# Kernel optimization log

Hardware: AMD Instinct MI355X
Metric: run time of the kernel (lower is better)

Reference implementation:

```python
import jax, jax.numpy as jnp
import numpy as np

N, NB, EU, ED, EB = 40000, 60000, 200000, 200000, 120000
D, H = 256, 256
BN_EPS = 1e-5


def _bn(x, g, b):
    # training-mode BatchNorm1d over the cell dimension (biased variance)
    mu = jnp.mean(x, axis=0)
    var = jnp.mean((x - mu) ** 2, axis=0)
    return g * (x - mu) * jax.lax.rsqrt(var + BN_EPS) + b


def _mlp(x, W1, b1, g1, c1, W2, b2, g2, c2):
    # update nn: Linear -> BN -> ReLU -> Linear -> BN -> ReLU
    h = jax.nn.relu(_bn(x @ W1 + b1, g1, c1))
    return jax.nn.relu(_bn(h @ W2 + b2, g2, c2))


def _forward(x, up_attr, down_attr, boundary_attr, Wmu, bmu, Wmd, bmd,
             W1u, b1u, g1u, c1u, W2u, b2u, g2u, c2u,
             W1d, b1d, g1d, c1d, W2d, b2d, g2d, c2d,
             W1b, b1b, g1b, c1b, W2b, b2b, g2b, c2b,
             Wc, bc, gc, cc, eps1, eps2, eps3,
             up_index, down_index, boundary_index):
    n, d = x.shape
    # msg_up_nn = ReLU(Linear(cat[x_j, up_attr])); split W to avoid materializing cat
    mu = jax.nn.relu(x[up_index[0]] @ Wmu[:d] + up_attr @ Wmu[d:] + bmu)
    agg_up = jax.ops.segment_sum(mu, up_index[1], num_segments=n)
    md = jax.nn.relu(x[down_index[0]] @ Wmd[:d] + down_attr @ Wmd[d:] + bmd)
    agg_down = jax.ops.segment_sum(md, down_index[1], num_segments=n)
    # msg_boundaries_nn is identity: gather boundary cell features, sum to targets
    agg_bnd = jax.ops.segment_sum(boundary_attr[boundary_index[0]], boundary_index[1], num_segments=n)
    out_up = _mlp(agg_up + (1.0 + eps1) * x, W1u, b1u, g1u, c1u, W2u, b2u, g2u, c2u)
    out_down = _mlp(agg_down + (1.0 + eps2) * x, W1d, b1d, g1d, c1d, W2d, b2d, g2d, c2d)
    out_bnd = _mlp(agg_bnd + (1.0 + eps3) * x, W1b, b1b, g1b, c1b, W2b, b2b, g2b, c2b)
    comb = jnp.concatenate([out_up, out_down, out_bnd], axis=-1)
    return jax.nn.relu(_bn(comb @ Wc + bc, gc, cc))


def setup_inputs() -> dict:
    key = jax.random.key(0)
    ks = iter(jax.random.split(key, 64))

    def nrm(shape, scale=1.0):
        return jax.random.normal(next(ks), shape, dtype=jnp.float32) * scale

    inp = {}
    inp['x'] = nrm((N, D))
    inp['up_attr'] = nrm((EU, D))
    inp['down_attr'] = nrm((ED, D))
    inp['boundary_attr'] = nrm((NB, D))
    s_msg = 1.0 / np.sqrt(2 * D)
    inp['Wmu'] = nrm((2 * D, D), s_msg); inp['bmu'] = jnp.zeros((D,), jnp.float32)
    inp['Wmd'] = nrm((2 * D, D), s_msg); inp['bmd'] = jnp.zeros((D,), jnp.float32)
    s1, s2 = 1.0 / np.sqrt(D), 1.0 / np.sqrt(H)
    for t in ('u', 'd', 'b'):
        inp['W1' + t] = nrm((D, H), s1); inp['b1' + t] = jnp.zeros((H,), jnp.float32)
        inp['g1' + t] = jnp.ones((H,), jnp.float32); inp['c1' + t] = jnp.zeros((H,), jnp.float32)
        inp['W2' + t] = nrm((H, H), s2); inp['b2' + t] = jnp.zeros((H,), jnp.float32)
        inp['g2' + t] = jnp.ones((H,), jnp.float32); inp['c2' + t] = jnp.zeros((H,), jnp.float32)
    inp['Wc'] = nrm((3 * H, H), 1.0 / np.sqrt(3 * H)); inp['bc'] = jnp.zeros((H,), jnp.float32)
    inp['gc'] = jnp.ones((H,), jnp.float32); inp['cc'] = jnp.zeros((H,), jnp.float32)
    inp['eps1'] = jnp.zeros((1,), jnp.float32)
    inp['eps2'] = jnp.zeros((1,), jnp.float32)
    inp['eps3'] = jnp.zeros((1,), jnp.float32)
    inp['up_index'] = jax.random.randint(next(ks), (2, EU), 0, N)
    inp['down_index'] = jax.random.randint(next(ks), (2, ED), 0, N)
    bsrc = jax.random.randint(next(ks), (EB,), 0, NB)
    btgt = jax.random.randint(next(ks), (EB,), 0, N)
    inp['boundary_index'] = jnp.stack([bsrc, btgt], axis=0)
    return inp


def reference(x, up_attr, down_attr, boundary_attr, Wmu, bmu, Wmd, bmd,
              W1u, b1u, g1u, c1u, W2u, b2u, g2u, c2u,
              W1d, b1d, g1d, c1d, W2d, b2d, g2d, c2d,
              W1b, b1b, g1b, c1b, W2b, b2b, g2b, c2b,
              Wc, bc, gc, cc, eps1, eps2, eps3,
              up_index, down_index, boundary_index):
    return _forward(x, up_attr, down_attr, boundary_attr, Wmu, bmu, Wmd, bmd,
                    W1u, b1u, g1u, c1u, W2u, b2u, g2u, c2u,
                    W1d, b1d, g1d, c1d, W2d, b2d, g2d, c2d,
                    W1b, b1b, g1b, c1b, W2b, b2b, g2b, c2b,
                    Wc, bc, gc, cc, eps1, eps2, eps3,
                    up_index, down_index, boundary_index)
```

## Files before the change

kernel.cpp:

```cpp
#include <hip/hip_runtime.h>
#include <hip/hip_bf16.h>
#include <stdint.h>

#define NCELL 40000
#define EUE   200000
#define EDE   200000
#define EBE   120000
#define NM    ((size_t)NCELL * 256)

typedef __attribute__((ext_vector_type(8))) short bf16x8;
typedef __attribute__((ext_vector_type(4))) float f32x4;

__device__ __forceinline__ uint16_t f2bf(float f) {
  union { float f; uint32_t u; } v; v.f = f;
  uint32_t u = v.u;
  u += 0x7fffu + ((u >> 16) & 1u);
  return (uint16_t)(u >> 16);
}

struct WArgs {
  const float* src[11];
  uint16_t*    dst[11];
  int          K[11];
};

__global__ void k_wconv(WArgs a) {
  int m = blockIdx.z;
  int K = a.K[m];
  int k0 = blockIdx.x * 32;
  if (k0 >= K) return;
  int n0 = blockIdx.y * 32;
  __shared__ float t[32][33];
  int tx = threadIdx.x, ty = threadIdx.y;
  const float* src = a.src[m];
  for (int i = ty; i < 32; i += 8)
    t[i][tx] = src[(size_t)(k0 + i) * 256 + n0 + tx];
  __syncthreads();
  uint16_t* dst = a.dst[m];
  for (int i = ty; i < 32; i += 8)
    dst[(size_t)(n0 + i) * K + k0 + tx] = f2bf(t[tx][i]);
}

__global__ void k_count(const int* __restrict__ tgt, int* __restrict__ cnt, int E) {
  int i = blockIdx.x * 256 + threadIdx.x;
  if (i < E) atomicAdd(&cnt[tgt[i]], 1);
}

struct ScanArgs { const int* cnt[3]; int* offs[3]; int* head[3]; };

__global__ void k_scan(ScanArgs a) {
  int s = blockIdx.x;
  const int n = NCELL;
  const int* cnt = a.cnt[s];
  int* offs = a.offs[s];
  int* head = a.head[s];
  __shared__ int buf[1024];
  __shared__ int carry;
  int tid = threadIdx.x;
  if (tid == 0) carry = 0;
  __syncthreads();
  for (int base = 0; base < n; base += 1024) {
    int i = base + tid;
    int v = (i < n) ? cnt[i] : 0;
    buf[tid] = v;
    __syncthreads();
    for (int d = 1; d < 1024; d <<= 1) {
      int t = (tid >= d) ? buf[tid - d] : 0;
      __syncthreads();
      buf[tid] += t;
      __syncthreads();
    }
    int excl = carry + buf[tid] - v;
    if (i < n) { offs[i] = excl; head[i] = excl; }
    __syncthreads();
    if (tid == 1023) carry += buf[1023];
    __syncthreads();
  }
  if (tid == 0) offs[n] = carry;
}

__global__ void k_fill(const int* __restrict__ src, const int* __restrict__ tgt,
                       int* __restrict__ head, int* __restrict__ perm,
                       int* __restrict__ psrc, int E) {
  int e = blockIdx.x * 256 + threadIdx.x;
  if (e < E) {
    int p = atomicAdd(&head[tgt[e]], 1);
    perm[p] = e;
    psrc[p] = src[e];
  }
}

__global__ void k_segsum(const float* __restrict__ MSG, const int* __restrict__ offs,
                         const int* __restrict__ perm, const float* __restrict__ x,
                         const float* __restrict__ eps, float* __restrict__ out) {
  int t = blockIdx.x * 4 + threadIdx.y;
  int c = threadIdx.x * 4;
  int s = offs[t], e = offs[t + 1];
  float sE = 1.f + *eps;
  float4 xa = *(const float4*)(x + (size_t)t * 256 + c);
  float a0 = xa.x * sE, a1 = xa.y * sE, a2 = xa.z * sE, a3 = xa.w * sE;
  int j = s;
  for (; j + 1 < e; j += 2) {
    int r0 = perm[j], r1 = perm[j + 1];
    float4 v0 = *(const float4*)(MSG + (size_t)r0 * 256 + c);
    float4 v1 = *(const float4*)(MSG + (size_t)r1 * 256 + c);
    a0 += v0.x + v1.x; a1 += v0.y + v1.y; a2 += v0.z + v1.z; a3 += v0.w + v1.w;
  }
  if (j < e) {
    int r0 = perm[j];
    float4 v0 = *(const float4*)(MSG + (size_t)r0 * 256 + c);
    a0 += v0.x; a1 += v0.y; a2 += v0.z; a3 += v0.w;
  }
  *(float4*)(out + (size_t)t * 256 + c) = make_float4(a0, a1, a2, a3);
}

__global__ void k_bgather(const float* __restrict__ battr, const int* __restrict__ offs,
                          const int* __restrict__ psrc, const float* __restrict__ x,
                          const float* __restrict__ eps, float* __restrict__ out) {
  int t = blockIdx.x * 4 + threadIdx.y;
  int c = threadIdx.x * 4;
  int s = offs[t], e = offs[t + 1];
  float sE = 1.f + *eps;
  float4 xa = *(const float4*)(x + (size_t)t * 256 + c);
  float a0 = xa.x * sE, a1 = xa.y * sE, a2 = xa.z * sE, a3 = xa.w * sE;
  int j = s;
  for (; j + 1 < e; j += 2) {
    int r0 = psrc[j], r1 = psrc[j + 1];
    float4 v0 = *(const float4*)(battr + (size_t)r0 * 256 + c);
    float4 v1 = *(const float4*)(battr + (size_t)r1 * 256 + c);
    a0 += v0.x + v1.x; a1 += v0.y + v1.y; a2 += v0.z + v1.z; a3 += v0.w + v1.w;
  }
  if (j < e) {
    int r0 = psrc[j];
    float4 v0 = *(const float4*)(battr + (size_t)r0 * 256 + c);
    a0 += v0.x; a1 += v0.y; a2 += v0.z; a3 += v0.w;
  }
  *(float4*)(out + (size_t)t * 256 + c) = make_float4(a0, a1, a2, a3);
}

__global__ void k_bnrelu(const float* __restrict__ Y, const float* __restrict__ s12,
                         const float* __restrict__ g, const float* __restrict__ cb,
                         float* __restrict__ out, int ldo) {
  int i = blockIdx.x * 256 + threadIdx.x;
  int c = (i & 63) * 4;
  size_t row = (size_t)(i >> 6);
  const float invN = 1.f / (float)NCELL;
  float4 v = *(const float4*)(Y + row * 256 + c);
  float vv[4] = {v.x, v.y, v.z, v.w};
  float o[4];
#pragma unroll
  for (int k = 0; k < 4; k++) {
    float mean = s12[c + k] * invN;
    float var  = s12[256 + c + k] * invN - mean * mean;
    float sc = g[c + k] * rsqrtf(var + 1e-5f);
    float sh = cb[c + k] - mean * sc;
    o[k] = fmaxf(vv[k] * sc + sh, 0.f);
  }
  *(float4*)(out + row * (size_t)ldo + c) = make_float4(o[0], o[1], o[2], o[3]);
}

struct CCArgs { const float* g[3]; const float* c[3]; float* Gg; float* Gc; };
__global__ void k_concat(CCArgs a) {
  int t = blockIdx.x, i = threadIdx.x;
  a.Gg[t * 256 + i] = a.g[t][i];
  a.Gc[t * 256 + i] = a.c[t][i];
}

template <int MODE, int FUSEBN>
__global__ __launch_bounds__(256)
void k_gemm(const float* __restrict__ A, const uint16_t* __restrict__ Bt, int K,
            const float* __restrict__ bias, float* __restrict__ C,
            float* __restrict__ stats, float* __restrict__ statsq,
            const float* __restrict__ bnS, const float* __restrict__ bnG,
            const float* __restrict__ bnC, const int* __restrict__ srcIdx,
            const float* __restrict__ XT, int M, int gx) {
  __shared__ uint16_t Al[128 * 32];
  __shared__ uint16_t Bl[128 * 32];
  const int tid = threadIdx.x;
  int id = blockIdx.x;
  int body2 = (gx & ~7) * 2;
  int m0, n0;
  if (id < body2) {
    int g = id >> 4, j = id & 15;
    m0 = ((g << 3) + (j & 7)) * 128;
    n0 = (j >> 3) * 128;
  } else {
    int r = id - body2, rem = gx & 7;
    m0 = ((gx & ~7) + (r % rem)) * 128;
    n0 = (r / rem) * 128;
  }
  const int lane = tid & 63;
  const int wave = tid >> 6;
  const int wr = (wave >> 1) * 64;
  const int wc = (wave & 1) * 64;
  const int lm = lane & 15;
  const int lq = lane >> 4;

  f32x4 acc[4][4];
#pragma unroll
  for (int i = 0; i < 4; i++)
#pragma unroll
    for (int j = 0; j < 4; j++)
      acc[i][j] = f32x4{0.f, 0.f, 0.f, 0.f};

  const int arow = tid >> 3;
  const int acol = (tid & 7) * 4;

  int pidx[4];
#pragma unroll
  for (int rr = 0; rr < 4; rr++) {
    int gr = m0 + arow + rr * 32;
    pidx[rr] = (gr < M) ? gr : -1;
  }

  const float invN = 1.f / (float)NCELL;
  for (int kt = 0; kt < K; kt += 32) {
    float sc[4], sh[4];
    if (FUSEBN) {
#pragma unroll
      for (int k2 = 0; k2 < 4; k2++) {
        int col = kt + acol + k2;
        float mean = bnS[col] * invN;
        float var  = bnS[K + col] * invN - mean * mean;
        float s = bnG[col] * rsqrtf(var + 1e-5f);
        sc[k2] = s; sh[k2] = bnC[col] - mean * s;
      }
    }
#pragma unroll
    for (int rr = 0; rr < 4; rr++) {
      int r = arow + rr * 32;
      float4 v = make_float4(0.f, 0.f, 0.f, 0.f);
      if (pidx[rr] >= 0) {
        const float* ap;
        if (MODE == 2) {
          int ct = kt + acol;
          ap = A + (size_t)(ct >> 8) * NM + (size_t)pidx[rr] * 256 + (ct & 255);
        } else {
          ap = A + (size_t)pidx[rr] * 256 + kt + acol;
        }
        v = *(const float4*)ap;
      }
      if (FUSEBN) {
        v.x = fmaxf(v.x * sc[0] + sh[0], 0.f);
        v.y = fmaxf(v.y * sc[1] + sh[1], 0.f);
        v.z = fmaxf(v.z * sc[2] + sh[2], 0.f);
        v.w = fmaxf(v.w * sc[3] + sh[3], 0.f);
      }
      union { uint16_t h[4]; uint2 u; } p;
      p.h[0] = f2bf(v.x); p.h[1] = f2bf(v.y); p.h[2] = f2bf(v.z); p.h[3] = f2bf(v.w);
      *(uint2*)(Al + r * 32 + acol) = p.u;
    }
#pragma unroll
    for (int ss = 0; ss < 2; ss++) {
      int j = tid + ss * 256;
      int row = j >> 2, kp = (j & 3) * 8;
      uint4 bv = *(const uint4*)(Bt + (size_t)(n0 + row) * K + kt + kp);
      *(uint4*)(Bl + row * 32 + kp) = bv;
    }
    __syncthreads();
    bf16x8 af[4], bfr[4];
#pragma unroll
    for (int i = 0; i < 4; i++)
      af[i] = *(const bf16x8*)(Al + (wr + 16 * i + lm) * 32 + lq * 8);
#pragma unroll
    for (int j = 0; j < 4; j++)
      bfr[j] = *(const bf16x8*)(Bl + (wc + 16 * j + lm) * 32 + lq * 8);
#pragma unroll
    for (int i = 0; i < 4; i++)
#pragma unroll
      for (int j = 0; j < 4; j++)
        acc[i][j] = __builtin_amdgcn_mfma_f32_16x16x32_bf16(af[i], bfr[j], acc[i][j], 0, 0, 0);
    __syncthreads();
  }

  const int cb0 = n0 + wc + lm;
  float bj[4];
#pragma unroll
  for (int j = 0; j < 4; j++) bj[j] = bias ? bias[cb0 + 16 * j] : 0.f;

  if (MODE == 1) {
#pragma unroll
    for (int i = 0; i < 4; i++) {
      int rbase = m0 + wr + 16 * i + lq * 4;
#pragma unroll
      for (int r = 0; r < 4; r++) {
        int row = rbase + r;
        if (row < M) {
          int sr = srcIdx[row];
          const float* xr = XT + (size_t)sr * 256;
#pragma unroll
          for (int j = 0; j < 4; j++) {
            float v = acc[i][j][r] + xr[cb0 + 16 * j] + bj[j];
            C[(size_t)row * 256 + cb0 + 16 * j] = fmaxf(v, 0.f);
          }
        }
      }
    }
  } else {
    float s1l[4] = {0.f, 0.f, 0.f, 0.f}, s2l[4] = {0.f, 0.f, 0.f, 0.f};
#pragma unroll
    for (int i = 0; i < 4; i++) {
      int rbase = m0 + wr + 16 * i + lq * 4;
#pragma unroll
      for (int r = 0; r < 4; r++) {
        int row = rbase + r;
        if (row < M) {
#pragma unroll
          for (int j = 0; j < 4; j++) {
            float v = acc[i][j][r] + bj[j];
            C[(size_t)row * 256 + cb0 + 16 * j] = v;
            s1l[j] += v;
            s2l[j] += v * v;
          }
        }
      }
    }
    if (stats) {
      float* sb0 = (float*)Al;
      float* sb1 = sb0 + 128;
      __syncthreads();
      sb0[tid] = 0.f;
      __syncthreads();
#pragma unroll
      for (int j = 0; j < 4; j++) {
        int colloc = wc + lm + 16 * j;
        atomicAdd(&sb0[colloc], s1l[j]);
        atomicAdd(&sb1[colloc], s2l[j]);
      }
      __syncthreads();
      if (tid < 128) {
        atomicAdd(&stats[n0 + tid],  sb0[tid]);
        atomicAdd(&statsq[n0 + tid], sb1[tid]);
      }
    }
  }
}

extern "C" void kernel_launch(void* const* d_in, const int* in_sizes, int n_in,
                              void* d_out, int out_size, void* d_ws, size_t ws_size,
                              hipStream_t stream) {
  const float* x    = (const float*)d_in[0];
  const float* upA  = (const float*)d_in[1];
  const float* dnA  = (const float*)d_in[2];
  const float* bA   = (const float*)d_in[3];
  const float* Wmu  = (const float*)d_in[4];
  const float* bmu  = (const float*)d_in[5];
  const float* Wmd  = (const float*)d_in[6];
  const float* bmd  = (const float*)d_in[7];
  const float* W1[3] = {(const float*)d_in[8],  (const float*)d_in[16], (const float*)d_in[24]};
  const float* b1[3] = {(const float*)d_in[9],  (const float*)d_in[17], (const float*)d_in[25]};
  const float* g1[3] = {(const float*)d_in[10], (const float*)d_in[18], (const float*)d_in[26]};
  const float* c1[3] = {(const float*)d_in[11], (const float*)d_in[19], (const float*)d_in[27]};
  const float* W2[3] = {(const float*)d_in[12], (const float*)d_in[20], (const float*)d_in[28]};
  const float* b2[3] = {(const float*)d_in[13], (const float*)d_in[21], (const float*)d_in[29]};
  const float* g2[3] = {(const float*)d_in[14], (const float*)d_in[22], (const float*)d_in[30]};
  const float* c2[3] = {(const float*)d_in[15], (const float*)d_in[23], (const float*)d_in[31]};
  const float* Wc   = (const float*)d_in[32];
  const float* bc   = (const float*)d_in[33];
  const float* gc   = (const float*)d_in[34];
  const float* cc   = (const float*)d_in[35];
  const float* e1   = (const float*)d_in[36];
  const float* e2   = (const float*)d_in[37];
  const float* e3   = (const float*)d_in[38];
  const int* upI = (const int*)d_in[39];
  const int* dnI = (const int*)d_in[40];
  const int* bI  = (const int*)d_in[41];

  float* base = (float*)d_ws;
  size_t o = 0;
  float* XU   = base + o; o += NM;
  float* XD   = base + o; o += NM;
  float* ACC0 = base + o; o += NM;
  float* ACC1 = base + o; o += NM;
  float* ACC2 = base + o; o += NM;
  float* POOL = base + o; o += 5 * NM;
  float* MSG  = POOL;
  float* Y3   = POOL;
  float* Y1   = POOL + 3 * NM;
  float* Yf   = POOL + 4 * NM;
  float* STATS = base + o; o += 3584;
  float* SCAT = STATS + 1536;
  float* SC   = STATS + 3072;
  float* GCg  = base + o; o += 768;
  float* GCc  = base + o; o += 768;
  uint16_t* wb = (uint16_t*)(base + o); o += 600000;
  uint16_t* WmuAt = wb;
  uint16_t* WmuBt = wb + 1 * 65536;
  uint16_t* WmdAt = wb + 2 * 65536;
  uint16_t* WmdBt = wb + 3 * 65536;
  uint16_t* W1t[3] = {wb + 4 * 65536, wb + 5 * 65536, wb + 6 * 65536};
  uint16_t* W2t[3] = {wb + 7 * 65536, wb + 8 * 65536, wb + 9 * 65536};
  uint16_t* Wct    = wb + 10 * 65536;
  int* ib = (int*)(base + o);
  int* offsU = ib;
  int* offsD = ib + 40001;
  int* offsB = ib + 80002;
  int* headU = ib + 120003;
  int* headD = ib + 160003;
  int* headB = ib + 200003;
  int* permU = ib + 240003;
  int* psrcU = ib + 440003;
  int* permD = ib + 640003;
  int* psrcD = ib + 840003;
  int* permB = ib + 1040003;
  int* psrcB = ib + 1160003;

  float* ACCs[3] = {ACC0, ACC1, ACC2};

  hipMemsetAsync(STATS, 0, 3584 * sizeof(float), stream);
  hipMemsetAsync(headU, 0, 3 * 40000 * sizeof(int), stream);

  WArgs wa;
  wa.src[0] = Wmu;               wa.dst[0] = WmuAt;  wa.K[0] = 256;
  wa.src[1] = Wmu + 256 * 256;   wa.dst[1] = WmuBt;  wa.K[1] = 256;
  wa.src[2] = Wmd;               wa.dst[2] = WmdAt;  wa.K[2] = 256;
  wa.src[3] = Wmd + 256 * 256;   wa.dst[3] = WmdBt;  wa.K[3] = 256;
  for (int t = 0; t < 3; t++) {
    wa.src[4 + 2 * t] = W1[t];   wa.dst[4 + 2 * t] = W1t[t]; wa.K[4 + 2 * t] = 256;
    wa.src[5 + 2 * t] = W2[t];   wa.dst[5 + 2 * t] = W2t[t]; wa.K[5 + 2 * t] = 256;
  }
  wa.src[10] = Wc; wa.dst[10] = Wct; wa.K[10] = 768;
  k_wconv<<<dim3(24, 8, 11), dim3(32, 8), 0, stream>>>(wa);

  CCArgs ca;
  for (int t = 0; t < 3; t++) { ca.g[t] = g2[t]; ca.c[t] = c2[t]; }
  ca.Gg = GCg; ca.Gc = GCc;
  k_concat<<<3, 256, 0, stream>>>(ca);

  k_count<<<(EUE + 255) / 256, 256, 0, stream>>>(upI + EUE, headU, EUE);
  k_count<<<(EDE + 255) / 256, 256, 0, stream>>>(dnI + EDE, headD, EDE);
  k_count<<<(EBE + 255) / 256, 256, 0, stream>>>(bI + EBE, headB, EBE);
  ScanArgs sa;
  sa.cnt[0] = headU; sa.offs[0] = offsU; sa.head[0] = headU;
  sa.cnt[1] = headD; sa.offs[1] = offsD; sa.head[1] = headD;
  sa.cnt[2] = headB; sa.offs[2] = offsB; sa.head[2] = headB;
  k_scan<<<3, 1024, 0, stream>>>(sa);
  k_fill<<<(EUE + 255) / 256, 256, 0, stream>>>(upI, upI + EUE, headU, permU, psrcU, EUE);
  k_fill<<<(EDE + 255) / 256, 256, 0, stream>>>(dnI, dnI + EDE, headD, permD, psrcD, EDE);
  k_fill<<<(EBE + 255) / 256, 256, 0, stream>>>(bI, bI + EBE, headB, permB, psrcB, EBE);

  const int gxN = (NCELL + 127) / 128;
  const int gxE = (EUE + 127) / 128;

  k_gemm<0, 0><<<gxN * 2, 256, 0, stream>>>(x, WmuAt, 256, nullptr, XU,
      nullptr, nullptr, nullptr, nullptr, nullptr, nullptr, nullptr, NCELL, gxN);
  k_gemm<0, 0><<<gxN * 2, 256, 0, stream>>>(x, WmdAt, 256, nullptr, XD,
      nullptr, nullptr, nullptr, nullptr, nullptr, nullptr, nullptr, NCELL, gxN);

  k_gemm<1, 0><<<gxE * 2, 256, 0, stream>>>(upA, WmuBt, 256, bmu, MSG,
      nullptr, nullptr, nullptr, nullptr, nullptr, upI, XU, EUE, gxE);
  k_segsum<<<10000, dim3(64, 4), 0, stream>>>(MSG, offsU, permU, x, e1, ACC0);

  k_gemm<1, 0><<<gxE * 2, 256, 0, stream>>>(dnA, WmdBt, 256, bmd, MSG,
      nullptr, nullptr, nullptr, nullptr, nullptr, dnI, XD, EDE, gxE);
  k_segsum<<<10000, dim3(64, 4), 0, stream>>>(MSG, offsD, permD, x, e2, ACC1);

  k_bgather<<<10000, dim3(64, 4), 0, stream>>>(bA, offsB, psrcB, x, e3, ACC2);

  for (int t = 0; t < 3; t++) {
    float* S1 = STATS + 512 * t;
    k_gemm<0, 0><<<gxN * 2, 256, 0, stream>>>(ACCs[t], W1t[t], 256, b1[t], Y1,
        S1, S1 + 256, nullptr, nullptr, nullptr, nullptr, nullptr, NCELL, gxN);
    k_gemm<0, 1><<<gxN * 2, 256, 0, stream>>>(Y1, W2t[t], 256, b2[t], Y3 + t * NM,
        SCAT + t * 256, SCAT + 768 + t * 256, S1, g1[t], c1[t], nullptr, nullptr, NCELL, gxN);
  }

  k_gemm<2, 1><<<gxN * 2, 256, 0, stream>>>(Y3, Wct, 768, bc, Yf,
      SC, SC + 256, SCAT, GCg, GCc, nullptr, nullptr, NCELL, gxN);
  k_bnrelu<<<10000, 256, 0, stream>>>(Yf, SC, gc, cc, (float*)d_out, 256);
}
```

Baseline: 1.489 ms.

## Store intermediates in half precision, double-buffer GEMM, batch launches over grid z

Intermediates (XU/XD, messages, aggregates, Y1, Y3) are now stored as fp16/bf16 instead of fp32. The GEMM gains double-buffered LDS with direct global-to-LDS loads. Parallel GEMMs and segment sums are batched into single launches using blockIdx.z or blockIdx.y, and the BN scale/shift is precomputed in a small prep kernel instead of inside every K-tile. The aim is to cut memory traffic and launch count, at the cost of lower precision in the stored intermediates.

```diff
diff --git a/kernel.cpp b/kernel.cpp
--- a/kernel.cpp
+++ b/kernel.cpp
@@ -1,5 +1,4 @@
 #include <hip/hip_runtime.h>
-#include <hip/hip_bf16.h>
 #include <stdint.h>
 
 #define NCELL 40000
@@ -16,6 +15,22 @@
   uint32_t u = v.u;
   u += 0x7fffu + ((u >> 16) & 1u);
   return (uint16_t)(u >> 16);
+}
+__device__ __forceinline__ float bf2f(uint16_t h) {
+  union { uint32_t u; float f; } v; v.u = (uint32_t)h << 16; return v.f;
+}
+__device__ __forceinline__ uint16_t f2h(float f) {
+  _Float16 h = (_Float16)f;
+  union { _Float16 h; uint16_t u; } v; v.h = h; return v.u;
+}
+__device__ __forceinline__ float h2f(uint16_t u) {
+  union { _Float16 h; uint16_t u; } v; v.u = u; return (float)v.h;
+}
+
+__device__ __forceinline__ void gll16(const void* g, void* l) {
+  __builtin_amdgcn_global_load_lds(
+      (const __attribute__((address_space(1))) uint32_t*)g,
+      (__attribute__((address_space(3))) uint32_t*)l, 16, 0, 0);
 }
 
 struct WArgs {
@@ -90,33 +105,49 @@
   }
 }
 
-__global__ void k_segsum(const float* __restrict__ MSG, const int* __restrict__ offs,
-                         const int* __restrict__ perm, const float* __restrict__ x,
-                         const float* __restrict__ eps, float* __restrict__ out) {
+struct SSArgs {
+  const uint16_t* msg[2]; const int* offs[2]; const int* perm[2];
+  const float* eps[2]; uint16_t* out[2]; const float* x;
+};
+
+__global__ void k_segsum2(SSArgs a) {
+  int z = blockIdx.y;
   int t = blockIdx.x * 4 + threadIdx.y;
   int c = threadIdx.x * 4;
+  const int* offs = a.offs[z];
+  const int* perm = a.perm[z];
+  const uint16_t* MSG = a.msg[z];
   int s = offs[t], e = offs[t + 1];
-  float sE = 1.f + *eps;
-  float4 xa = *(const float4*)(x + (size_t)t * 256 + c);
+  float sE = 1.f + *a.eps[z];
+  float4 xa = *(const float4*)(a.x + (size_t)t * 256 + c);
   float a0 = xa.x * sE, a1 = xa.y * sE, a2 = xa.z * sE, a3 = xa.w * sE;
   int j = s;
   for (; j + 1 < e; j += 2) {
     int r0 = perm[j], r1 = perm[j + 1];
-    float4 v0 = *(const float4*)(MSG + (size_t)r0 * 256 + c);
-    float4 v1 = *(const float4*)(MSG + (size_t)r1 * 256 + c);
-    a0 += v0.x + v1.x; a1 += v0.y + v1.y; a2 += v0.z + v1.z; a3 += v0.w + v1.w;
+    uint2 v0 = *(const uint2*)(MSG + (size_t)r0 * 256 + c);
+    uint2 v1 = *(const uint2*)(MSG + (size_t)r1 * 256 + c);
+    a0 += h2f((uint16_t)v0.x) + h2f((uint16_t)v1.x);
+    a1 += h2f((uint16_t)(v0.x >> 16)) + h2f((uint16_t)(v1.x >> 16));
+    a2 += h2f((uint16_t)v0.y) + h2f((uint16_t)v1.y);
+    a3 += h2f((uint16_t)(v0.y >> 16)) + h2f((uint16_t)(v1.y >> 16));
   }
   if (j < e) {
     int r0 = perm[j];
-    float4 v0 = *(const float4*)(MSG + (size_t)r0 * 256 + c);
-    a0 += v0.x; a1 += v0.y; a2 += v0.z; a3 += v0.w;
-  }
-  *(float4*)(out + (size_t)t * 256 + c) = make_float4(a0, a1, a2, a3);
+    uint2 v0 = *(const uint2*)(MSG + (size_t)r0 * 256 + c);
+    a0 += h2f((uint16_t)v0.x);
+    a1 += h2f((uint16_t)(v0.x >> 16));
+    a2 += h2f((uint16_t)v0.y);
+    a3 += h2f((uint16_t)(v0.y >> 16));
+  }
+  uint2 ov;
+  ov.x = (uint32_t)f2bf(a0) | ((uint32_t)f2bf(a1) << 16);
+  ov.y = (uint32_t)f2bf(a2) | ((uint32_t)f2bf(a3) << 16);
+  *(uint2*)(a.out[z] + (size_t)t * 256 + c) = ov;
 }
 
 __global__ void k_bgather(const float* __restrict__ battr, const int* __restrict__ offs,
                           const int* __restrict__ psrc, const float* __restrict__ x,
-                          const float* __restrict__ eps, float* __restrict__ out) {
+                          const float* __restrict__ eps, uint16_t* __restrict__ out) {
   int t = blockIdx.x * 4 + threadIdx.y;
   int c = threadIdx.x * 4;
   int s = offs[t], e = offs[t + 1];
@@ -135,7 +166,26 @@
     float4 v0 = *(const float4*)(battr + (size_t)r0 * 256 + c);
     a0 += v0.x; a1 += v0.y; a2 += v0.z; a3 += v0.w;
   }
-  *(float4*)(out + (size_t)t * 256 + c) = make_float4(a0, a1, a2, a3);
+  uint2 ov;
+  ov.x = (uint32_t)f2bf(a0) | ((uint32_t)f2bf(a1) << 16);
+  ov.y = (uint32_t)f2bf(a2) | ((uint32_t)f2bf(a3) << 16);
+  *(uint2*)(out + (size_t)t * 256 + c) = ov;
+}
+
+struct BPArgs {
+  const float* st[3]; const float* sq[3];
+  const float* g[3];  const float* c[3];
+  float* sc; float* sh;
+};
+
+__global__ void k_bnprep(BPArgs a) {
+  int z = blockIdx.x, i = threadIdx.x;
+  const float invN = 1.f / (float)NCELL;
+  float mean = a.st[z][i] * invN;
+  float var  = a.sq[z][i] * invN - mean * mean;
+  float s = a.g[z][i] * rsqrtf(var + 1e-5f);
+  a.sc[z * 256 + i] = s;
+  a.sh[z * 256 + i] = a.c[z][i] - mean * s;
 }
 
 __global__ void k_bnrelu(const float* __restrict__ Y, const float* __restrict__ s12,
@@ -159,24 +209,26 @@
   *(float4*)(out + row * (size_t)ldo + c) = make_float4(o[0], o[1], o[2], o[3]);
 }
 
-struct CCArgs { const float* g[3]; const float* c[3]; float* Gg; float* Gc; };
-__global__ void k_concat(CCArgs a) {
-  int t = blockIdx.x, i = threadIdx.x;
-  a.Gg[t * 256 + i] = a.g[t][i];
-  a.Gc[t * 256 + i] = a.c[t][i];
-}
-
-template <int MODE, int FUSEBN>
+struct GArgs {
+  const void* A[3];
+  const uint16_t* B[3];
+  const float* bias[3];
+  void* C[3];
+  float* st[3]; float* stq[3];
+  const float* sc[3]; const float* sh[3];
+  const int* srcIdx[3];
+  const uint16_t* XT[3];
+  int M, K, gx;
+};
+
+template <int MODE, int AF32, int FUSEBN, int CF32>
 __global__ __launch_bounds__(256)
-void k_gemm(const float* __restrict__ A, const uint16_t* __restrict__ Bt, int K,
-            const float* __restrict__ bias, float* __restrict__ C,
-            float* __restrict__ stats, float* __restrict__ statsq,
-            const float* __restrict__ bnS, const float* __restrict__ bnG,
-            const float* __restrict__ bnC, const int* __restrict__ srcIdx,
-            const float* __restrict__ XT, int M, int gx) {
-  __shared__ uint16_t Al[128 * 32];
-  __shared__ uint16_t Bl[128 * 32];
+void k_gemm(GArgs a) {
+  __shared__ uint16_t Al[2][128 * 32];
+  __shared__ uint16_t Bl[2][128 * 32];
+  const int z = blockIdx.z;
   const int tid = threadIdx.x;
+  const int gx = a.gx;
   int id = blockIdx.x;
   int body2 = (gx & ~7) * 2;
   int m0, n0;
@@ -189,12 +241,11 @@
     m0 = ((gx & ~7) + (r % rem)) * 128;
     n0 = (r / rem) * 128;
   }
-  const int lane = tid & 63;
-  const int wave = tid >> 6;
-  const int wr = (wave >> 1) * 64;
-  const int wc = (wave & 1) * 64;
-  const int lm = lane & 15;
-  const int lq = lane >> 4;
+  const int lane = tid & 63, wave = tid >> 6;
+  const int wr = (wave >> 1) * 64, wc = (wave & 1) * 64;
+  const int lm = lane & 15, lq = lane >> 4;
+  const int M = a.M, K = a.K;
+  const uint16_t* Bt = a.B[z];
 
   f32x4 acc[4][4];
 #pragma unroll
@@ -205,80 +256,139 @@
 
   const int arow = tid >> 3;
   const int acol = (tid & 7) * 4;
-
-  int pidx[4];
-#pragma unroll
-  for (int rr = 0; rr < 4; rr++) {
-    int gr = m0 + arow + rr * 32;
-    pidx[rr] = (gr < M) ? gr : -1;
-  }
-
-  const float invN = 1.f / (float)NCELL;
-  for (int kt = 0; kt < K; kt += 32) {
-    float sc[4], sh[4];
-    if (FUSEBN) {
-#pragma unroll
-      for (int k2 = 0; k2 < 4; k2++) {
-        int col = kt + acol + k2;
-        float mean = bnS[col] * invN;
-        float var  = bnS[K + col] * invN - mean * mean;
-        float s = bnG[col] * rsqrtf(var + 1e-5f);
-        sc[k2] = s; sh[k2] = bnC[col] - mean * s;
+  const int srow = tid >> 2;
+  const int sc8  = (tid & 3) * 8;
+
+  const float* Af = (const float*)a.A[z];
+  const uint16_t* Ah = (const uint16_t*)a.A[z];
+  const uint16_t* A3_0 = (const uint16_t*)a.A[0];
+  const uint16_t* A3_1 = (const uint16_t*)a.A[1];
+  const uint16_t* A3_2 = (const uint16_t*)a.A[2];
+  const float* scp = a.sc[z];
+  const float* shp = a.sh[z];
+
+  f32x4 av[4];
+  uint4 ah[2];
+  f32x4 scv[2][2], shv[2][2];
+
+  auto issueB = [&](int b, int ktc) {
+#pragma unroll
+    for (int ss = 0; ss < 2; ss++) {
+      int row = srow + ss * 64;
+      gll16(Bt + (size_t)(n0 + row) * K + ktc + sc8,
+            (uint16_t*)Bl[b] + (size_t)(wave * 64 + ss * 256) * 8);
+    }
+  };
+  auto issueAg = [&](int b, int ktc) {
+#pragma unroll
+    for (int ss = 0; ss < 2; ss++) {
+      int row = srow + ss * 64;
+      gll16(Ah + (size_t)(m0 + row) * 256 + ktc + sc8,
+            (uint16_t*)Al[b] + (size_t)(wave * 64 + ss * 256) * 8);
+    }
+  };
+  auto issueA32 = [&](int ktc) {
+#pragma unroll
+    for (int rr = 0; rr < 4; rr++) {
+      int gr = m0 + arow + rr * 32;
+      av[rr] = f32x4{0.f, 0.f, 0.f, 0.f};
+      if (gr < M) av[rr] = *(const f32x4*)(Af + (size_t)gr * 256 + ktc + acol);
+    }
+  };
+  auto writeA32 = [&](int b) {
+#pragma unroll
+    for (int rr = 0; rr < 4; rr++) {
+      uint32_t lo = (uint32_t)f2bf(av[rr][0]) | ((uint32_t)f2bf(av[rr][1]) << 16);
+      uint32_t hi = (uint32_t)f2bf(av[rr][2]) | ((uint32_t)f2bf(av[rr][3]) << 16);
+      uint2 p; p.x = lo; p.y = hi;
+      *(uint2*)&Al[b][(arow + rr * 32) * 32 + acol] = p;
+    }
+  };
+  auto issueAF = [&](int ktc) {
+#pragma unroll
+    for (int ss = 0; ss < 2; ss++) {
+      int row = srow + ss * 64;
+      int ct = ktc + sc8;
+      const uint16_t* src;
+      if (MODE == 2) {
+        int ch = ktc >> 8;
+        const uint16_t* sel = (ch == 0) ? A3_0 : (ch == 1 ? A3_1 : A3_2);
+        src = sel + (size_t)(m0 + row) * 256 + (ct & 255);
+      } else {
+        src = Ah + (size_t)(m0 + row) * 256 + ct;
       }
-    }
-#pragma unroll
-    for (int rr = 0; rr < 4; rr++) {
-      int r = arow + rr * 32;
-      float4 v = make_float4(0.f, 0.f, 0.f, 0.f);
-      if (pidx[rr] >= 0) {
-        const float* ap;
-        if (MODE == 2) {
-          int ct = kt + acol;
-          ap = A + (size_t)(ct >> 8) * NM + (size_t)pidx[rr] * 256 + (ct & 255);
-        } else {
-          ap = A + (size_t)pidx[rr] * 256 + kt + acol;
-        }
-        v = *(const float4*)ap;
-      }
-      if (FUSEBN) {
-        v.x = fmaxf(v.x * sc[0] + sh[0], 0.f);
-        v.y = fmaxf(v.y * sc[1] + sh[1], 0.f);
-        v.z = fmaxf(v.z * sc[2] + sh[2], 0.f);
-        v.w = fmaxf(v.w * sc[3] + sh[3], 0.f);
-      }
-      union { uint16_t h[4]; uint2 u; } p;
-      p.h[0] = f2bf(v.x); p.h[1] = f2bf(v.y); p.h[2] = f2bf(v.z); p.h[3] = f2bf(v.w);
-      *(uint2*)(Al + r * 32 + acol) = p.u;
-    }
+      ah[ss] = *(const uint4*)src;
+      scv[ss][0] = *(const f32x4*)(scp + ct);
+      scv[ss][1] = *(const f32x4*)(scp + ct + 4);
+      shv[ss][0] = *(const f32x4*)(shp + ct);
+      shv[ss][1] = *(const f32x4*)(shp + ct + 4);
+    }
+  };
+  auto proc2 = [&](uint32_t w, float s0, float h0, float s1, float h1) -> uint32_t {
+    float v0 = fmaxf(h2f((uint16_t)w) * s0 + h0, 0.f);
+    float v1 = fmaxf(h2f((uint16_t)(w >> 16)) * s1 + h1, 0.f);
+    return (uint32_t)f2bf(v0) | ((uint32_t)f2bf(v1) << 16);
+  };
+  auto writeAF = [&](int b) {
 #pragma unroll
     for (int ss = 0; ss < 2; ss++) {
-      int j = tid + ss * 256;
-      int row = j >> 2, kp = (j & 3) * 8;
-      uint4 bv = *(const uint4*)(Bt + (size_t)(n0 + row) * K + kt + kp);
-      *(uint4*)(Bl + row * 32 + kp) = bv;
-    }
-    __syncthreads();
+      int row = srow + ss * 64;
+      uint4 o;
+      o.x = proc2(ah[ss].x, scv[ss][0][0], shv[ss][0][0], scv[ss][0][1], shv[ss][0][1]);
+      o.y = proc2(ah[ss].y, scv[ss][0][2], shv[ss][0][2], scv[ss][0][3], shv[ss][0][3]);
+      o.z = proc2(ah[ss].z, scv[ss][1][0], shv[ss][1][0], scv[ss][1][1], shv[ss][1][1]);
+      o.w = proc2(ah[ss].w, scv[ss][1][2], shv[ss][1][2], scv[ss][1][3], shv[ss][1][3]);
+      *(uint4*)&Al[b][row * 32 + sc8] = o;
+    }
+  };
+
+  const int NT = K >> 5;
+  issueB(0, 0);
+  if constexpr (AF32)        { issueA32(0); writeA32(0); }
+  else if constexpr (FUSEBN) { issueAF(0);  writeAF(0);  }
+  else                       issueAg(0, 0);
+  __syncthreads();
+
+  int cur = 0;
+  for (int T = 0; T < NT; T++) {
+    bool more = (T + 1 < NT);
+    int nk = (T + 1) << 5;
+    if (more) {
+      issueB(cur ^ 1, nk);
+      if constexpr (AF32)        issueA32(nk);
+      else if constexpr (FUSEBN) issueAF(nk);
+      else                       issueAg(cur ^ 1, nk);
+    }
     bf16x8 af[4], bfr[4];
 #pragma unroll
     for (int i = 0; i < 4; i++)
-      af[i] = *(const bf16x8*)(Al + (wr + 16 * i + lm) * 32 + lq * 8);
+      af[i] = *(const bf16x8*)&Al[cur][(wr + 16 * i + lm) * 32 + lq * 8];
 #pragma unroll
     for (int j = 0; j < 4; j++)
-      bfr[j] = *(const bf16x8*)(Bl + (wc + 16 * j + lm) * 32 + lq * 8);
+      bfr[j] = *(const bf16x8*)&Bl[cur][(wc + 16 * j + lm) * 32 + lq * 8];
 #pragma unroll
     for (int i = 0; i < 4; i++)
 #pragma unroll
       for (int j = 0; j < 4; j++)
         acc[i][j] = __builtin_amdgcn_mfma_f32_16x16x32_bf16(af[i], bfr[j], acc[i][j], 0, 0, 0);
+    if (more) {
+      if constexpr (AF32)        writeA32(cur ^ 1);
+      else if constexpr (FUSEBN) writeAF(cur ^ 1);
+    }
     __syncthreads();
+    cur ^= 1;
   }
 
   const int cb0 = n0 + wc + lm;
+  const float* bias = a.bias[z];
   float bj[4];
 #pragma unroll
   for (int j = 0; j < 4; j++) bj[j] = bias ? bias[cb0 + 16 * j] : 0.f;
 
-  if (MODE == 1) {
+  if constexpr (MODE == 1) {
+    const int* sidx = a.srcIdx[z];
+    const uint16_t* XTz = a.XT[z];
+    uint16_t* Cz = (uint16_t*)a.C[z];
 #pragma unroll
     for (int i = 0; i < 4; i++) {
       int rbase = m0 + wr + 16 * i + lq * 4;
@@ -286,18 +396,20 @@
       for (int r = 0; r < 4; r++) {
         int row = rbase + r;
         if (row < M) {
-          int sr = srcIdx[row];
-          const float* xr = XT + (size_t)sr * 256;
+          int sr = sidx[row];
+          const uint16_t* xr = XTz + (size_t)sr * 256;
 #pragma unroll
           for (int j = 0; j < 4; j++) {
-            float v = acc[i][j][r] + xr[cb0 + 16 * j] + bj[j];
-            C[(size_t)row * 256 + cb0 + 16 * j] = fmaxf(v, 0.f);
+            float v = acc[i][j][r] + h2f(xr[cb0 + 16 * j]) + bj[j];
+            Cz[(size_t)row * 256 + cb0 + 16 * j] = f2h(fmaxf(v, 0.f));
           }
         }
       }
     }
   } else {
     float s1l[4] = {0.f, 0.f, 0.f, 0.f}, s2l[4] = {0.f, 0.f, 0.f, 0.f};
+    float* Cf = (float*)a.C[z];
+    uint16_t* Ch = (uint16_t*)a.C[z];
 #pragma unroll
     for (int i = 0; i < 4; i++) {
       int rbase = m0 + wr + 16 * i + lq * 4;
@@ -308,14 +420,15 @@
 #pragma unroll
           for (int j = 0; j < 4; j++) {
             float v = acc[i][j][r] + bj[j];
-            C[(size_t)row * 256 + cb0 + 16 * j] = v;
+            if constexpr (CF32) Cf[(size_t)row * 256 + cb0 + 16 * j] = v;
+            else                Ch[(size_t)row * 256 + cb0 + 16 * j] = f2h(v);
             s1l[j] += v;
             s2l[j] += v * v;
           }
         }
       }
     }
-    if (stats) {
+    if (a.st[z]) {
       float* sb0 = (float*)Al;
       float* sb1 = sb0 + 128;
       __syncthreads();
@@ -329,8 +442,8 @@
       }
       __syncthreads();
       if (tid < 128) {
-        atomicAdd(&stats[n0 + tid],  sb0[tid]);
-        atomicAdd(&statsq[n0 + tid], sb1[tid]);
+        atomicAdd(&a.st[z][n0 + tid],  sb0[tid]);
+        atomicAdd(&a.stq[z][n0 + tid], sb1[tid]);
       }
     }
   }
@@ -368,21 +481,20 @@
 
   float* base = (float*)d_ws;
   size_t o = 0;
-  float* XU   = base + o; o += NM;
-  float* XD   = base + o; o += NM;
-  float* ACC0 = base + o; o += NM;
-  float* ACC1 = base + o; o += NM;
-  float* ACC2 = base + o; o += NM;
+  uint16_t* XUb = (uint16_t*)(base + o); o += NM / 2;
+  uint16_t* XDb = (uint16_t*)(base + o); o += NM / 2;
+  uint16_t* ACCb[3];
+  for (int t = 0; t < 3; t++) { ACCb[t] = (uint16_t*)(base + o); o += NM / 2; }
   float* POOL = base + o; o += 5 * NM;
-  float* MSG  = POOL;
-  float* Y3   = POOL;
-  float* Y1   = POOL + 3 * NM;
-  float* Yf   = POOL + 4 * NM;
+  uint16_t* MSGb[2] = {(uint16_t*)POOL, (uint16_t*)(POOL + 5 * NM / 2)};
+  uint16_t* Y1b = (uint16_t*)POOL;
+  uint16_t* Y3b = (uint16_t*)(POOL + 3 * NM / 2);
+  float* Yf = POOL + 3 * NM;
   float* STATS = base + o; o += 3584;
   float* SCAT = STATS + 1536;
-  float* SC   = STATS + 3072;
-  float* GCg  = base + o; o += 768;
-  float* GCc  = base + o; o += 768;
+  float* SCp  = STATS + 3072;
+  float* SCSH1 = base + o; o += 1536;
+  float* SCSH2 = base + o; o += 1536;
   uint16_t* wb = (uint16_t*)(base + o); o += 600000;
   uint16_t* WmuAt = wb;
   uint16_t* WmuBt = wb + 1 * 65536;
@@ -405,8 +517,6 @@
   int* permB = ib + 1040003;
   int* psrcB = ib + 1160003;
 
-  float* ACCs[3] = {ACC0, ACC1, ACC2};
-
   hipMemsetAsync(STATS, 0, 3584 * sizeof(float), stream);
   hipMemsetAsync(headU, 0, 3 * 40000 * sizeof(int), stream);
 
@@ -421,11 +531,6 @@
   }
   wa.src[10] = Wc; wa.dst[10] = Wct; wa.K[10] = 768;
   k_wconv<<<dim3(24, 8, 11), dim3(32, 8), 0, stream>>>(wa);
-
-  CCArgs ca;
-  for (int t = 0; t < 3; t++) { ca.g[t] = g2[t]; ca.c[t] = c2[t]; }
-  ca.Gg = GCg; ca.Gc = GCc;
-  k_concat<<<3, 256, 0, stream>>>(ca);
 
   k_count<<<(EUE + 255) / 256, 256, 0, stream>>>(upI + EUE, headU, EUE);
   k_count<<<(EDE + 255) / 256, 256, 0, stream>>>(dnI + EDE, headD, EDE);
@@ -442,30 +547,98 @@
   const int gxN = (NCELL + 127) / 128;
   const int gxE = (EUE + 127) / 128;
 
-  k_gemm<0, 0><<<gxN * 2, 256, 0, stream>>>(x, WmuAt, 256, nullptr, XU,
-      nullptr, nullptr, nullptr, nullptr, nullptr, nullptr, nullptr, NCELL, gxN);
-  k_gemm<0, 0><<<gxN * 2, 256, 0, stream>>>(x, WmdAt, 256, nullptr, XD,
-      nullptr, nullptr, nullptr, nullptr, nullptr, nullptr, nullptr, NCELL, gxN);
-
-  k_gemm<1, 0><<<gxE * 2, 256, 0, stream>>>(upA, WmuBt, 256, bmu, MSG,
-      nullptr, nullptr, nullptr, nullptr, nullptr, upI, XU, EUE, gxE);
-  k_segsum<<<10000, dim3(64, 4), 0, stream>>>(MSG, offsU, permU, x, e1, ACC0);
-
-  k_gemm<1, 0><<<gxE * 2, 256, 0, stream>>>(dnA, WmdBt, 256, bmd, MSG,
-      nullptr, nullptr, nullptr, nullptr, nullptr, dnI, XD, EDE, gxE);
-  k_segsum<<<10000, dim3(64, 4), 0, stream>>>(MSG, offsD, permD, x, e2, ACC1);
-
-  k_bgather<<<10000, dim3(64, 4), 0, stream>>>(bA, offsB, psrcB, x, e3, ACC2);
-
-  for (int t = 0; t < 3; t++) {
-    float* S1 = STATS + 512 * t;
-    k_gemm<0, 0><<<gxN * 2, 256, 0, stream>>>(ACCs[t], W1t[t], 256, b1[t], Y1,
-        S1, S1 + 256, nullptr, nullptr, nullptr, nullptr, nullptr, NCELL, gxN);
-    k_gemm<0, 1><<<gxN * 2, 256, 0, stream>>>(Y1, W2t[t], 256, b2[t], Y3 + t * NM,
-        SCAT + t * 256, SCAT + 768 + t * 256, S1, g1[t], c1[t], nullptr, nullptr, NCELL, gxN);
-  }
-
-  k_gemm<2, 1><<<gxN * 2, 256, 0, stream>>>(Y3, Wct, 768, bc, Yf,
-      SC, SC + 256, SCAT, GCg, GCc, nullptr, nullptr, NCELL, gxN);
-  k_bnrelu<<<10000, 256, 0, stream>>>(Yf, SC, gc, cc, (float*)d_out, 256);
-}
+  {
+    GArgs g{};
+    g.A[0] = x; g.A[1] = x;
+    g.B[0] = WmuAt; g.B[1] = WmdAt;
+    g.C[0] = XUb; g.C[1] = XDb;
+    g.M = NCELL; g.K = 256; g.gx = gxN;
+    k_gemm<0, 1, 0, 0><<<dim3(gxN * 2, 1, 2), 256, 0, stream>>>(g);
+  }
+
+  {
+    GArgs g{};
+    g.A[0] = upA; g.A[1] = dnA;
+    g.B[0] = WmuBt; g.B[1] = WmdBt;
+    g.bias[0] = bmu; g.bias[1] = bmd;
+    g.C[0] = MSGb[0]; g.C[1] = MSGb[1];
+    g.srcIdx[0] = upI; g.srcIdx[1] = dnI;
+    g.XT[0] = XUb; g.XT[1] = XDb;
+    g.M = EUE; g.K = 256; g.gx = gxE;
+    k_gemm<1, 1, 0, 0><<<dim3(gxE * 2, 1, 2), 256, 0, stream>>>(g);
+  }
+
+  {
+    SSArgs s{};
+    s.msg[0] = MSGb[0]; s.msg[1] = MSGb[1];
+    s.offs[0] = offsU;  s.offs[1] = offsD;
+    s.perm[0] = permU;  s.perm[1] = permD;
+    s.eps[0] = e1;      s.eps[1] = e2;
+    s.out[0] = ACCb[0]; s.out[1] = ACCb[1];
+    s.x = x;
+    k_segsum2<<<dim3(10000, 2), dim3(64, 4), 0, stream>>>(s);
+  }
+
+  k_bgather<<<10000, dim3(64, 4), 0, stream>>>(bA, offsB, psrcB, x, e3, ACCb[2]);
+
+  {
+    GArgs g{};
+    for (int t = 0; t < 3; t++) {
+      g.A[t] = ACCb[t];
+      g.B[t] = W1t[t];
+      g.bias[t] = b1[t];
+      g.C[t] = Y1b + (size_t)t * NM;
+      g.st[t] = STATS + 512 * t; g.stq[t] = STATS + 512 * t + 256;
+    }
+    g.M = NCELL; g.K = 256; g.gx = gxN;
+    k_gemm<0, 0, 0, 0><<<dim3(gxN * 2, 1, 3), 256, 0, stream>>>(g);
+  }
+
+  {
+    BPArgs b{};
+    for (int t = 0; t < 3; t++) {
+      b.st[t] = STATS + 512 * t; b.sq[t] = STATS + 512 * t + 256;
+      b.g[t] = g1[t]; b.c[t] = c1[t];
+    }
+    b.sc = SCSH1; b.sh = SCSH1 + 768;
+    k_bnprep<<<3, 256, 0, stream>>>(b);
+  }
+
+  {
+    GArgs g{};
+    for (int t = 0; t < 3; t++) {
+      g.A[t] = Y1b + (size_t)t * NM;
+      g.B[t] = W2t[t];
+      g.bias[t] = b2[t];
+      g.C[t] = Y3b + (size_t)t * NM;
+      g.st[t] = SCAT + 256 * t; g.stq[t] = SCAT + 768 + 256 * t;
+      g.sc[t] = SCSH1 + 256 * t; g.sh[t] = SCSH1 + 768 + 256 * t;
+    }
+    g.M = NCELL; g.K = 256; g.gx = gxN;
+    k_gemm<0, 0, 1, 0><<<dim3(gxN * 2, 1, 3), 256, 0, stream>>>(g);
+  }
+
+  {
+    BPArgs b{};
+    for (int t = 0; t < 3; t++) {
+      b.st[t] = SCAT + 256 * t; b.sq[t] = SCAT + 768 + 256 * t;
+      b.g[t] = g2[t]; b.c[t] = c2[t];
+    }
+    b.sc = SCSH2; b.sh = SCSH2 + 768;
+    k_bnprep<<<3, 256, 0, stream>>>(b);
+  }
+
+  {
+    GArgs g{};
+    g.A[0] = Y3b; g.A[1] = Y3b + NM; g.A[2] = Y3b + 2 * NM;
+    g.B[0] = Wct;
+    g.bias[0] = bc;
+    g.C[0] = Yf;
+    g.st[0] = SCp; g.stq[0] = SCp + 256;
+    g.sc[0] = SCSH2; g.sh[0] = SCSH2 + 768;
+    g.M = NCELL; g.K = 768; g.gx = gxN;
+    k_gemm<2, 0, 1, 1><<<dim3(gxN * 2, 1, 1), 256, 0, stream>>>(g);
+  }
+
+  k_bnrelu<<<10000, 256, 0, stream>>>(Yf, SCp, gc, cc, (float*)d_out, 256);
+}
```

Measured after the change: 1.457 ms. 2.2% less time.
